# Kernel tuning notes

Hardware: AMD Instinct MI355X
Metric: run time of the kernel (lower is better)

## Reference

```python
import jax, jax.numpy as jnp
import numpy as np
from jax.scipy.special import xlogy

N = 8_388_608   # B*L flattened tokens
NCATS = 3       # genotype classes 0/1/2
GROUP = 4       # minimac r2 group size
IGNORE = -100


def setup_inputs() -> dict:
    key = jax.random.key(0)
    k1, k2 = jax.random.split(key)
    logits = jax.random.normal(k1, (N, NCATS), dtype=jnp.float32)
    targets = jax.random.randint(k2, (N,), 0, NCATS, dtype=jnp.int32)
    return {"logits": logits, "targets": targets}


def reference(logits, targets):
    log_probs = jax.nn.log_softmax(logits, axis=-1)          # (N, C)
    probs = jnp.exp(log_probs)                               # (N, C)

    valid = targets != IGNORE                                # (N,)
    tgt = jnp.where(valid, targets, 0)

    # CrossEntropyLoss(ignore_index, reduction='sum')
    picked = jnp.take_along_axis(log_probs, tgt[:, None], axis=-1)[:, 0]
    ce_loss = -jnp.sum(jnp.where(valid, picked, 0.0))

    # KLDivLoss(reduction='sum')(log_probs, probs) = sum probs*(log(probs) - log_probs)
    kl_loss = jnp.sum(xlogy(probs, probs) - probs * log_probs)

    # minimac R2 over groups of GROUP consecutive *valid* rows (L == 1).
    alt_p = 1.0 - probs[:, 0]                                # (N,)
    af = tgt.astype(jnp.float32) / 2.0
    edge = (af == 0.0) | (af == 1.0)                         # mask in _r2
    af2 = jnp.where(edge, 0.5, af)
    denom = jnp.maximum(af2 * (1.0 - af2), 0.01)
    sq = (alt_p - af2) ** 2

    w = valid.astype(jnp.float32)
    rank = jnp.cumsum(valid.astype(jnp.int32)) - valid.astype(jnp.int32)
    gid = rank // GROUP                                       # group id among valid rows
    num_groups = N // GROUP + 1

    cnt = jax.ops.segment_sum(w, gid, num_segments=num_groups)         # group sizes
    ssq = jax.ops.segment_sum(sq * w, gid, num_segments=num_groups)
    mse = ssq / jnp.maximum(cnt, 1.0)                                  # per-group mean

    # per-element: where(edge, 0, mse_g/denom); group contribution scaled by cnt_g
    term = w * jnp.where(edge, 0.0, mse[gid] / denom) * cnt[gid]
    r2_loss = -jnp.sum(term)

    return ce_loss + kl_loss + r2_loss
```

## Files before the change

### kernel.cpp

```cpp
#include <hip/hip_runtime.h>


constexpr int IGNORE_IDX = -100;

#define NBLOCKS1 2048
#define THREADS1 256

__device__ __forceinline__ float group_term(const float4& a, const float4& b,
                                            const float4& c, const int4& t4) {
    float L[4][3] = {
        {a.x, a.y, a.z},
        {a.w, b.x, b.y},
        {b.z, b.w, c.x},
        {c.y, c.z, c.w},
    };
    int T[4] = {t4.x, t4.y, t4.z, t4.w};

    float ce  = 0.0f;
    float ssq = 0.0f;
    float n1  = 0.0f;

    #pragma unroll
    for (int j = 0; j < 4; ++j) {
        float l0 = L[j][0], l1 = L[j][1], l2 = L[j][2];
        float m  = fmaxf(l0, fmaxf(l1, l2));
        float e0 = __expf(l0 - m);
        float e1 = __expf(l1 - m);
        float e2 = __expf(l2 - m);
        float s  = e0 + e1 + e2;
        float lse = m + __logf(s);

        int  t = T[j];
        bool v = (t != IGNORE_IDX);
        float lt = (t == 1) ? l1 : ((t == 2) ? l2 : l0);
        if (v) {
            ce += lse - lt;
            float p0 = e0 * __builtin_amdgcn_rcpf(s);
            float d  = 0.5f - p0;
            ssq += d * d;
            if (t == 1) n1 += 1.0f;
        }
    }
    return ce - 4.0f * ssq * n1;
}

__global__ __launch_bounds__(THREADS1) void imp_loss_stage1(
    const float* __restrict__ logits,
    const int*   __restrict__ targets,
    float*       __restrict__ partials,
    int ngroups)
{
    const int tid    = blockIdx.x * blockDim.x + threadIdx.x;
    const int stride = gridDim.x * blockDim.x;

    float local = 0.0f;
    int gid = tid;

    for (; gid + 3 * stride < ngroups; gid += 4 * stride) {
        float4 A[4], B[4], C[4];
        int4   T4[4];
        #pragma unroll
        for (int k = 0; k < 4; ++k) {
            const int g = gid + k * stride;
            const float4* lg = reinterpret_cast<const float4*>(logits) + (size_t)g * 3;
            A[k] = lg[0];
            B[k] = lg[1];
            C[k] = lg[2];
            T4[k] = reinterpret_cast<const int4*>(targets)[g];
        }
        #pragma unroll
        for (int k = 0; k < 4; ++k)
            local += group_term(A[k], B[k], C[k], T4[k]);
    }

    for (; gid < ngroups; gid += stride) {
        const float4* lg = reinterpret_cast<const float4*>(logits) + (size_t)gid * 3;
        float4 a = lg[0], b = lg[1], c = lg[2];
        int4 t4 = reinterpret_cast<const int4*>(targets)[gid];
        local += group_term(a, b, c, t4);
    }

    #pragma unroll
    for (int off = 32; off > 0; off >>= 1)
        local += __shfl_down(local, off, 64);

    __shared__ float wsum[THREADS1 / 64];
    const int lane = threadIdx.x & 63;
    const int wid  = threadIdx.x >> 6;
    if (lane == 0) wsum[wid] = local;
    __syncthreads();
    if (threadIdx.x == 0) {
        float s = 0.0f;
        #pragma unroll
        for (int w = 0; w < THREADS1 / 64; ++w) s += wsum[w];
        partials[blockIdx.x] = s;
    }
}

__global__ __launch_bounds__(256) void imp_loss_stage2(
    const float* __restrict__ partials,
    float*       __restrict__ out,
    int n)
{
    float local = 0.0f;
    for (int i = threadIdx.x; i < n; i += 256)
        local += partials[i];

    #pragma unroll
    for (int off = 32; off > 0; off >>= 1)
        local += __shfl_down(local, off, 64);

    __shared__ float wsum[4];
    const int lane = threadIdx.x & 63;
    const int wid  = threadIdx.x >> 6;
    if (lane == 0) wsum[wid] = local;
    __syncthreads();
    if (threadIdx.x == 0)
        out[0] = wsum[0] + wsum[1] + wsum[2] + wsum[3];
}

extern "C" void kernel_launch(void* const* d_in, const int* in_sizes, int n_in,
                              void* d_out, int out_size, void* d_ws, size_t ws_size,
                              hipStream_t stream) {
    const float* logits  = (const float*)d_in[0];
    const int*   targets = (const int*)d_in[1];
    float* out      = (float*)d_out;
    float* partials = (float*)d_ws;

    const int N = in_sizes[1];
    const int ngroups = N / 4;

    imp_loss_stage1<<<NBLOCKS1, THREADS1, 0, stream>>>(logits, targets, partials, ngroups);
    imp_loss_stage2<<<1, 256, 0, stream>>>(partials, out, NBLOCKS1);
}
```

Before: 173.1 us.

## Fuse final reduction via last-block atomic counter and use nontemporal loads

Replaces the separate second-stage reduction kernel with a last-block-done pattern: each block writes its partial, fences, increments an atomic counter, and the final block sums all partials. A memset of the counter is added before the launch. Input loads switch to nontemporal loads to avoid polluting cache with streaming data. This trades one kernel launch for a memset plus an atomic and fence per block.

```diff
diff --git a/kernel.cpp b/kernel.cpp
--- a/kernel.cpp
+++ b/kernel.cpp
@@ -6,8 +6,11 @@
 #define NBLOCKS1 2048
 #define THREADS1 256
 
-__device__ __forceinline__ float group_term(const float4& a, const float4& b,
-                                            const float4& c, const int4& t4) {
+typedef float fx4 __attribute__((ext_vector_type(4)));
+typedef int   ix4 __attribute__((ext_vector_type(4)));
+
+__device__ __forceinline__ float group_term(const fx4& a, const fx4& b,
+                                            const fx4& c, const ix4& t4) {
     float L[4][3] = {
         {a.x, a.y, a.z},
         {a.w, b.x, b.y},
@@ -44,29 +47,34 @@
     return ce - 4.0f * ssq * n1;
 }
 
-__global__ __launch_bounds__(THREADS1) void imp_loss_stage1(
+__global__ __launch_bounds__(THREADS1) void imp_loss_fused(
     const float* __restrict__ logits,
     const int*   __restrict__ targets,
+    float*       __restrict__ out,
     float*       __restrict__ partials,
+    unsigned int* __restrict__ counter,
     int ngroups)
 {
     const int tid    = blockIdx.x * blockDim.x + threadIdx.x;
-    const int stride = gridDim.x * blockDim.x;
+    const int stride = NBLOCKS1 * THREADS1;
+
+    const fx4* __restrict__ lg4 = reinterpret_cast<const fx4*>(logits);
+    const ix4* __restrict__ tg4 = reinterpret_cast<const ix4*>(targets);
 
     float local = 0.0f;
     int gid = tid;
 
     for (; gid + 3 * stride < ngroups; gid += 4 * stride) {
-        float4 A[4], B[4], C[4];
-        int4   T4[4];
+        fx4 A[4], B[4], C[4];
+        ix4 T4[4];
         #pragma unroll
         for (int k = 0; k < 4; ++k) {
             const int g = gid + k * stride;
-            const float4* lg = reinterpret_cast<const float4*>(logits) + (size_t)g * 3;
-            A[k] = lg[0];
-            B[k] = lg[1];
-            C[k] = lg[2];
-            T4[k] = reinterpret_cast<const int4*>(targets)[g];
+            const fx4* lg = lg4 + (size_t)g * 3;
+            A[k]  = __builtin_nontemporal_load(lg);
+            B[k]  = __builtin_nontemporal_load(lg + 1);
+            C[k]  = __builtin_nontemporal_load(lg + 2);
+            T4[k] = __builtin_nontemporal_load(tg4 + g);
         }
         #pragma unroll
         for (int k = 0; k < 4; ++k)
@@ -74,9 +82,11 @@
     }
 
     for (; gid < ngroups; gid += stride) {
-        const float4* lg = reinterpret_cast<const float4*>(logits) + (size_t)gid * 3;
-        float4 a = lg[0], b = lg[1], c = lg[2];
-        int4 t4 = reinterpret_cast<const int4*>(targets)[gid];
+        const fx4* lg = lg4 + (size_t)gid * 3;
+        fx4 a = __builtin_nontemporal_load(lg);
+        fx4 b = __builtin_nontemporal_load(lg + 1);
+        fx4 c = __builtin_nontemporal_load(lg + 2);
+        ix4 t4 = __builtin_nontemporal_load(tg4 + gid);
         local += group_term(a, b, c, t4);
     }
 
@@ -85,38 +95,40 @@
         local += __shfl_down(local, off, 64);
 
     __shared__ float wsum[THREADS1 / 64];
+    __shared__ bool  amLast;
     const int lane = threadIdx.x & 63;
     const int wid  = threadIdx.x >> 6;
     if (lane == 0) wsum[wid] = local;
     __syncthreads();
+
     if (threadIdx.x == 0) {
         float s = 0.0f;
         #pragma unroll
         for (int w = 0; w < THREADS1 / 64; ++w) s += wsum[w];
         partials[blockIdx.x] = s;
+        __threadfence();
+        unsigned int prev = atomicAdd(counter, 1u);
+        amLast = (prev == (unsigned int)(gridDim.x - 1));
     }
-}
+    __syncthreads();
 
-__global__ __launch_bounds__(256) void imp_loss_stage2(
-    const float* __restrict__ partials,
-    float*       __restrict__ out,
-    int n)
-{
-    float local = 0.0f;
-    for (int i = threadIdx.x; i < n; i += 256)
-        local += partials[i];
-
-    #pragma unroll
-    for (int off = 32; off > 0; off >>= 1)
-        local += __shfl_down(local, off, 64);
-
-    __shared__ float wsum[4];
-    const int lane = threadIdx.x & 63;
-    const int wid  = threadIdx.x >> 6;
-    if (lane == 0) wsum[wid] = local;
-    __syncthreads();
-    if (threadIdx.x == 0)
-        out[0] = wsum[0] + wsum[1] + wsum[2] + wsum[3];
+    if (amLast) {
+        float s = 0.0f;
+        for (int i = threadIdx.x; i < NBLOCKS1; i += THREADS1)
+            s += __hip_atomic_load(&partials[i], __ATOMIC_RELAXED,
+                                   __HIP_MEMORY_SCOPE_AGENT);
+        #pragma unroll
+        for (int off = 32; off > 0; off >>= 1)
+            s += __shfl_down(s, off, 64);
+        if (lane == 0) wsum[wid] = s;
+        __syncthreads();
+        if (threadIdx.x == 0) {
+            float tot = 0.0f;
+            #pragma unroll
+            for (int w = 0; w < THREADS1 / 64; ++w) tot += wsum[w];
+            out[0] = tot;
+        }
+    }
 }
 
 extern "C" void kernel_launch(void* const* d_in, const int* in_sizes, int n_in,
@@ -124,12 +136,15 @@
                               hipStream_t stream) {
     const float* logits  = (const float*)d_in[0];
     const int*   targets = (const int*)d_in[1];
-    float* out      = (float*)d_out;
-    float* partials = (float*)d_ws;
+    float* out = (float*)d_out;
+
+    unsigned int* counter  = (unsigned int*)d_ws;
+    float*        partials = (float*)((char*)d_ws + 256);
 
     const int N = in_sizes[1];
     const int ngroups = N / 4;
 
-    imp_loss_stage1<<<NBLOCKS1, THREADS1, 0, stream>>>(logits, targets, partials, ngroups);
-    imp_loss_stage2<<<1, 256, 0, stream>>>(partials, out, NBLOCKS1);
+    (void)hipMemsetAsync(counter, 0, sizeof(unsigned int), stream);
+    imp_loss_fused<<<NBLOCKS1, THREADS1, 0, stream>>>(logits, targets, out,
+                                                      partials, counter, ngroups);
 }
```

Result: slower. 272.9 us (+57.7%).
